# Performance work log

Measured on AMD Instinct MI355X. Metric: run time of the kernel, lower is better.

Reference implementation:

```python
import jax, jax.numpy as jnp
import numpy as np

B, N, C, H = 16, 1029, 1024, 16
D = C // H  # head_dim = 64
N_ROPE = 1024  # patch tokens covered by rope; prefix = N - N_ROPE = 5


def setup_inputs() -> dict:
    key = jax.random.key(0)
    ks = jax.random.split(key, 8)
    x = jax.random.normal(ks[0], (B, N, C), dtype=jnp.float32)
    rope_sin = jax.random.uniform(ks[1], (N_ROPE, D), dtype=jnp.float32, minval=-1.0, maxval=1.0)
    rope_cos = jax.random.uniform(ks[2], (N_ROPE, D), dtype=jnp.float32, minval=-1.0, maxval=1.0)
    s = 1.0 / np.sqrt(C)
    W_qkv = jax.random.normal(ks[3], (3 * C, C), dtype=jnp.float32) * s
    b_qkv = jax.random.normal(ks[4], (3 * C,), dtype=jnp.float32) * 0.02
    W_proj = jax.random.normal(ks[5], (C, C), dtype=jnp.float32) * s
    b_proj = jax.random.normal(ks[6], (C,), dtype=jnp.float32) * 0.02
    return {"x": x, "rope_sin": rope_sin, "rope_cos": rope_cos,
            "W_qkv": W_qkv, "b_qkv": b_qkv, "W_proj": W_proj, "b_proj": b_proj}


def _rotate_half(t):
    t1, t2 = jnp.split(t, 2, axis=-1)
    return jnp.concatenate([-t2, t1], axis=-1)


def _rope_apply(t, sin, cos):
    # t: [B, H, N_rope, D]; sin/cos: [N_rope, D] broadcast over B, H
    return t * cos + _rotate_half(t) * sin


def reference(x, rope_sin, rope_cos, W_qkv, b_qkv, W_proj, b_proj):
    b, n, c = x.shape
    h, d = H, c // H
    # QKV projection (torch Linear: x @ W.T + b)
    qkv = x @ W_qkv.T + b_qkv                       # [B, N, 3C]
    qkv = qkv.reshape(b, n, 3, h, d)
    q = jnp.transpose(qkv[:, :, 0], (0, 2, 1, 3))   # [B, H, N, D]
    k = jnp.transpose(qkv[:, :, 1], (0, 2, 1, 3))
    v = jnp.transpose(qkv[:, :, 2], (0, 2, 1, 3))
    # RoPE on the patch-token suffix only
    prefix = n - rope_sin.shape[-2]
    q = jnp.concatenate([q[:, :, :prefix], _rope_apply(q[:, :, prefix:], rope_sin, rope_cos)], axis=2)
    k = jnp.concatenate([k[:, :, :prefix], _rope_apply(k[:, :, prefix:], rope_sin, rope_cos)], axis=2)
    # Scaled dot-product attention (default scale = 1/sqrt(D))
    scale = 1.0 / jnp.sqrt(jnp.asarray(d, dtype=x.dtype))
    scores = jnp.einsum('bhqd,bhkd->bhqk', q, k) * scale
    attn = jax.nn.softmax(scores, axis=-1)
    out = jnp.einsum('bhqk,bhkd->bhqd', attn, v)    # [B, H, N, D]
    out = jnp.transpose(out, (0, 2, 1, 3)).reshape(b, n, c)
    # Output projection
    return out @ W_proj.T + b_proj
```

## Files before the change

kernel.cpp:

```cpp
#include <hip/hip_runtime.h>
#include <cfloat>
#include <math.h>

#define B_      16
#define N_TOK   1029
#define C_      1024
#define H_      16
#define D_      64
#define PREFIX  5
#define M_ROWS  (B_ * N_TOK)
#define HEAD_SLAB ((size_t)B_ * H_ * N_TOK * D_)
#define VT_STRIDE 1088

typedef __attribute__((ext_vector_type(8))) short bf16x8;
typedef __attribute__((ext_vector_type(4))) float f32x4;

__device__ __forceinline__ unsigned short f2bf(float f) {
    unsigned u = __float_as_uint(f);
    u += 0x7fffu + ((u >> 16) & 1u);
    return (unsigned short)(u >> 16);
}
__device__ __forceinline__ float bf2f(unsigned short h) {
    return __uint_as_float(((unsigned)h) << 16);
}

__global__ __launch_bounds__(256)
void split_kernel(const float* __restrict__ in, unsigned short* __restrict__ hi,
                  unsigned short* __restrict__ lo, int n4)
{
    const int i = blockIdx.x * 256 + threadIdx.x;
    if (i >= n4) return;
    const float4 v = ((const float4*)in)[i];
    ushort4 h, l;
    h.x = f2bf(v.x); l.x = f2bf(v.x - bf2f(h.x));
    h.y = f2bf(v.y); l.y = f2bf(v.y - bf2f(h.y));
    h.z = f2bf(v.z); l.z = f2bf(v.z - bf2f(h.z));
    h.w = f2bf(v.w); l.w = f2bf(v.w - bf2f(h.w));
    ((ushort4*)hi)[i] = h;
    ((ushort4*)lo)[i] = l;
}

__global__ __launch_bounds__(256)
void gemm_mfma(const unsigned short* __restrict__ Ahi, const unsigned short* __restrict__ Alo,
               const unsigned short* __restrict__ Whi, const unsigned short* __restrict__ Wlo,
               const float* __restrict__ bias, float* __restrict__ out,
               int M, int Ncols, int K, int scatter)
{
    __shared__ unsigned short lds[4][128 * 32];

    const int tid  = threadIdx.x;
    const int wave = tid >> 6;
    const int lane = tid & 63;
    const int bx = blockIdx.x, by = blockIdx.y;
    const int wm = wave >> 1, wn = wave & 1;

    f32x4 acc[4][4];
#pragma unroll
    for (int mi = 0; mi < 4; ++mi)
#pragma unroll
        for (int ni = 0; ni < 4; ++ni)
            acc[mi][ni] = (f32x4){0.f, 0.f, 0.f, 0.f};

    const unsigned short* src = (wave == 0) ? Ahi : (wave == 1) ? Alo
                              : (wave == 2) ? Whi : Wlo;
    const bool isA  = (wave < 2);
    const int  row0 = isA ? by * 128 : bx * 128;
    const int  rlo  = lane >> 2;
    const int  koff = (lane & 3) << 3;

    const int lm = lane & 15;
    const int q8 = (lane >> 4) << 3;

    for (int k0 = 0; k0 < K; k0 += 32) {
        __syncthreads();
#pragma unroll
        for (int i = 0; i < 8; ++i) {
            int grow = row0 + i * 16 + rlo;
            if (isA && grow > M - 1) grow = M - 1;
            const unsigned short* g = src + (size_t)grow * K + k0 + koff;
            __builtin_amdgcn_global_load_lds(
                (__attribute__((address_space(1))) void*)g,
                (__attribute__((address_space(3))) void*)&lds[wave][i * 512],
                16, 0, 0);
        }
        __syncthreads();

        bf16x8 ah[4], al[4], bh[4], bl[4];
#pragma unroll
        for (int mi = 0; mi < 4; ++mi) {
            const int r = wm * 64 + mi * 16 + lm;
            ah[mi] = *(const bf16x8*)&lds[0][r * 32 + q8];
            al[mi] = *(const bf16x8*)&lds[1][r * 32 + q8];
        }
#pragma unroll
        for (int ni = 0; ni < 4; ++ni) {
            const int r = wn * 64 + ni * 16 + lm;
            bh[ni] = *(const bf16x8*)&lds[2][r * 32 + q8];
            bl[ni] = *(const bf16x8*)&lds[3][r * 32 + q8];
        }
#pragma unroll
        for (int mi = 0; mi < 4; ++mi)
#pragma unroll
            for (int ni = 0; ni < 4; ++ni) {
                acc[mi][ni] = __builtin_amdgcn_mfma_f32_16x16x32_bf16(ah[mi], bh[ni], acc[mi][ni], 0, 0, 0);
                acc[mi][ni] = __builtin_amdgcn_mfma_f32_16x16x32_bf16(ah[mi], bl[ni], acc[mi][ni], 0, 0, 0);
                acc[mi][ni] = __builtin_amdgcn_mfma_f32_16x16x32_bf16(al[mi], bh[ni], acc[mi][ni], 0, 0, 0);
            }
    }

    const int quad = lane >> 4;
#pragma unroll
    for (int mi = 0; mi < 4; ++mi) {
#pragma unroll
        for (int r = 0; r < 4; ++r) {
            const int gm = by * 128 + wm * 64 + mi * 16 + quad * 4 + r;
            if (gm >= M) continue;
            if (!scatter) {
#pragma unroll
                for (int ni = 0; ni < 4; ++ni) {
                    const int gn = bx * 128 + wn * 64 + ni * 16 + lm;
                    out[(size_t)gm * Ncols + gn] = acc[mi][ni][r] + bias[gn];
                }
            } else {
                const int b   = gm / N_TOK;
                const int tok = gm - b * N_TOK;
#pragma unroll
                for (int ni = 0; ni < 4; ++ni) {
                    const int gn    = bx * 128 + wn * 64 + ni * 16 + lm;
                    const int which = gn >> 10;
                    const int h     = (gn >> 6) & 15;
                    const int d     = gn & 63;
                    const size_t dst = (size_t)which * HEAD_SLAB +
                                       (((size_t)(b * H_ + h)) * N_TOK + tok) * 64 + d;
                    out[dst] = acc[mi][ni][r] + bias[gn];
                }
            }
        }
    }
}

__global__ __launch_bounds__(256)
void rope_convert(const float* __restrict__ qf, const float* __restrict__ kf,
                  const float* __restrict__ sin_, const float* __restrict__ cos_,
                  unsigned short* __restrict__ qhi, unsigned short* __restrict__ qlo,
                  unsigned short* __restrict__ khi, unsigned short* __restrict__ klo)
{
    const int idx = blockIdx.x * 256 + threadIdx.x;
    const int total = B_ * H_ * N_TOK * 32;
    if (idx >= total) return;
    const int d   = idx & 31;
    const int tmp = idx >> 5;
    const int n   = tmp % N_TOK;
    const int bh  = tmp / N_TOK;

    const size_t base = ((size_t)bh * N_TOK + n) * 64;
    float q1 = qf[base + d], q2 = qf[base + d + 32];
    float k1 = kf[base + d], k2 = kf[base + d + 32];

    if (n >= PREFIX) {
        const int r = n - PREFIX;
        const float c1 = cos_[r * 64 + d];
        const float c2 = cos_[r * 64 + d + 32];
        const float s1 = sin_[r * 64 + d];
        const float s2 = sin_[r * 64 + d + 32];
        const float nq1 = q1 * c1 - q2 * s1;
        const float nq2 = q2 * c2 + q1 * s2;
        q1 = nq1; q2 = nq2;
        const float nk1 = k1 * c1 - k2 * s1;
        const float nk2 = k2 * c2 + k1 * s2;
        k1 = nk1; k2 = nk2;
    }
    q1 *= 0.125f; q2 *= 0.125f;

    unsigned short h;
    h = f2bf(q1); qhi[base + d]      = h; qlo[base + d]      = f2bf(q1 - bf2f(h));
    h = f2bf(q2); qhi[base + d + 32] = h; qlo[base + d + 32] = f2bf(q2 - bf2f(h));
    h = f2bf(k1); khi[base + d]      = h; klo[base + d]      = f2bf(k1 - bf2f(h));
    h = f2bf(k2); khi[base + d + 32] = h; klo[base + d + 32] = f2bf(k2 - bf2f(h));
}

__global__ __launch_bounds__(256)
void v_transpose(const float* __restrict__ vf, unsigned short* __restrict__ vt)
{
    __shared__ float t[64][65];
    const int tid = threadIdx.x;
    const int kt0 = blockIdx.x * 64;
    const int bh  = blockIdx.y;
    const float* src = vf + (size_t)bh * N_TOK * 64;

#pragma unroll
    for (int p = 0; p < 4; ++p) {
        const int e   = p * 256 + tid;
        const int key = e >> 4;
        const int c4  = (e & 15) << 2;
        const int gk  = kt0 + key;
        float4 v = make_float4(0.f, 0.f, 0.f, 0.f);
        if (gk < N_TOK) v = *(const float4*)(src + (size_t)gk * 64 + c4);
        t[key][c4 + 0] = v.x;
        t[key][c4 + 1] = v.y;
        t[key][c4 + 2] = v.z;
        t[key][c4 + 3] = v.w;
    }
    __syncthreads();

    const int d  = tid >> 2;
    const int kb = (tid & 3) << 4;
    unsigned short buf[16];
#pragma unroll
    for (int j = 0; j < 16; ++j) buf[j] = f2bf(t[kb + j][d]);
    unsigned short* dst = vt + (size_t)bh * 64 * VT_STRIDE + (size_t)d * VT_STRIDE + kt0 + kb;
#pragma unroll
    for (int j = 0; j < 4; ++j)
        *(ushort4*)(dst + j * 4) = *(ushort4*)&buf[j * 4];
}

__global__ __launch_bounds__(256, 2)
void attn_mfma2(const unsigned short* __restrict__ qhi_g, const unsigned short* __restrict__ qlo_g,
                const unsigned short* __restrict__ khi_g, const unsigned short* __restrict__ klo_g,
                const unsigned short* __restrict__ vt_g,
                unsigned short* __restrict__ Ohi, unsigned short* __restrict__ Olo)
{
    __shared__ unsigned short Khl[2][64 * 64];
    __shared__ unsigned short Kll[2][64 * 64];
    __shared__ unsigned short Vtl[2][64 * 64];
    __shared__ unsigned short Pl[128 * 64];

    const int tid  = threadIdx.x;
    const int wave = tid >> 6;
    const int lane = tid & 63;
    const int lm   = lane & 15;
    const int quad = lane >> 4;
    const int bh   = blockIdx.x;
    const int q0   = blockIdx.y * 128;
    const int b    = bh >> 4;
    const int h    = bh & 15;

    const unsigned short* Qh  = qhi_g + (size_t)bh * N_TOK * 64;
    const unsigned short* Ql  = qlo_g + (size_t)bh * N_TOK * 64;
    const unsigned short* Khb = khi_g + (size_t)bh * N_TOK * 64;
    const unsigned short* Klb = klo_g + (size_t)bh * N_TOK * 64;
    const unsigned short* Vtb = vt_g  + (size_t)bh * 64 * VT_STRIDE;

#define STAGE(bs, kt0_) do {                                                     \
    _Pragma("unroll")                                                            \
    for (int pass = 0; pass < 2; ++pass) {                                       \
        const int t  = pass * 256 + tid;                                         \
        const int r  = t >> 3;                                                   \
        const int qs = t & 7;                                                    \
        const int sw = (qs ^ (r & 7)) << 3;                                      \
        const int ldsoff = (pass * 256 + wave * 64) * 8;                         \
        const int gk = min((kt0_) + r, N_TOK - 1);                               \
        __builtin_amdgcn_global_load_lds(                                        \
            (__attribute__((address_space(1))) void*)(Khb + (size_t)gk * 64 + sw), \
            (__attribute__((address_space(3))) void*)&Khl[bs][ldsoff], 16, 0, 0);  \
        __builtin_amdgcn_global_load_lds(                                        \
            (__attribute__((address_space(1))) void*)(Klb + (size_t)gk * 64 + sw), \
            (__attribute__((address_space(3))) void*)&Kll[bs][ldsoff], 16, 0, 0);  \
        __builtin_amdgcn_global_load_lds(                                        \
            (__attribute__((address_space(1))) void*)(Vtb + (size_t)r * VT_STRIDE + (kt0_) + sw), \
            (__attribute__((address_space(3))) void*)&Vtl[bs][ldsoff], 16, 0, 0);  \
    }                                                                            \
} while (0)

    STAGE(0, 0);

    bf16x8 qh[2][2], ql[2][2];
#pragma unroll
    for (int rt = 0; rt < 2; ++rt) {
        int row = q0 + wave * 32 + rt * 16 + lm;
        if (row > N_TOK - 1) row = N_TOK - 1;
#pragma unroll
        for (int s = 0; s < 2; ++s) {
            const size_t off = (size_t)row * 64 + s * 32 + quad * 8;
            qh[rt][s] = *(const bf16x8*)&Qh[off];
            ql[rt][s] = *(const bf16x8*)&Ql[off];
        }
    }

    f32x4 o[2][4];
    float m_i[2][4], l_i[2][4];
#pragma unroll
    for (int rt = 0; rt < 2; ++rt)
#pragma unroll
        for (int r = 0; r < 4; ++r) {
            m_i[rt][r] = -FLT_MAX;
            l_i[rt][r] = 0.f;
            o[rt][r] = (f32x4){0.f, 0.f, 0.f, 0.f};
        }

    asm volatile("s_waitcnt vmcnt(0)\n\ts_barrier" ::: "memory");

    for (int kt = 0; kt < 17; ++kt) {
        const int kt0 = kt * 64;
        const int cur = kt & 1;

        if (kt < 16) STAGE(cur ^ 1, kt0 + 64);

        f32x4 s_acc[2][4];
#pragma unroll
        for (int rt = 0; rt < 2; ++rt)
#pragma unroll
            for (int ct = 0; ct < 4; ++ct)
                s_acc[rt][ct] = (f32x4){0.f, 0.f, 0.f, 0.f};

#pragma unroll
        for (int ct = 0; ct < 4; ++ct) {
            const int krow = ct * 16 + lm;
#pragma unroll
            for (int s = 0; s < 2; ++s) {
                const int chunk = ((s * 4 + quad) ^ (krow & 7)) << 3;
                const bf16x8 kbh = *(const bf16x8*)&Khl[cur][krow * 64 + chunk];
                const bf16x8 kbl = *(const bf16x8*)&Kll[cur][krow * 64 + chunk];
#pragma unroll
                for (int rt = 0; rt < 2; ++rt) {
                    s_acc[rt][ct] = __builtin_amdgcn_mfma_f32_16x16x32_bf16(qh[rt][s], kbh, s_acc[rt][ct], 0, 0, 0);
                    s_acc[rt][ct] = __builtin_amdgcn_mfma_f32_16x16x32_bf16(qh[rt][s], kbl, s_acc[rt][ct], 0, 0, 0);
                    s_acc[rt][ct] = __builtin_amdgcn_mfma_f32_16x16x32_bf16(ql[rt][s], kbh, s_acc[rt][ct], 0, 0, 0);
                }
            }
        }

        if (kt0 + 64 > N_TOK) {
#pragma unroll
            for (int ct = 0; ct < 4; ++ct) {
                if (kt0 + ct * 16 + lm >= N_TOK) {
#pragma unroll
                    for (int rt = 0; rt < 2; ++rt)
#pragma unroll
                        for (int r = 0; r < 4; ++r) s_acc[rt][ct][r] = -FLT_MAX;
                }
            }
        }

#pragma unroll
        for (int rt = 0; rt < 2; ++rt) {
#pragma unroll
            for (int r = 0; r < 4; ++r) {
                float mt = fmaxf(fmaxf(s_acc[rt][0][r], s_acc[rt][1][r]),
                                 fmaxf(s_acc[rt][2][r], s_acc[rt][3][r]));
                mt = fmaxf(mt, __shfl_xor(mt, 1));
                mt = fmaxf(mt, __shfl_xor(mt, 2));
                mt = fmaxf(mt, __shfl_xor(mt, 4));
                mt = fmaxf(mt, __shfl_xor(mt, 8));
                const float mnew  = fmaxf(m_i[rt][r], mt);
                const float alpha = __expf(m_i[rt][r] - mnew);
                float pv[4], rs = 0.f;
#pragma unroll
                for (int ct = 0; ct < 4; ++ct) {
                    pv[ct] = __expf(s_acc[rt][ct][r] - mnew);
                    rs += pv[ct];
                }
                rs += __shfl_xor(rs, 1);
                rs += __shfl_xor(rs, 2);
                rs += __shfl_xor(rs, 4);
                rs += __shfl_xor(rs, 8);
                l_i[rt][r] = l_i[rt][r] * alpha + rs;
                m_i[rt][r] = mnew;
#pragma unroll
                for (int dt = 0; dt < 4; ++dt) o[rt][dt][r] *= alpha;
                const int prow = wave * 32 + rt * 16 + quad * 4 + r;
#pragma unroll
                for (int ct = 0; ct < 4; ++ct) {
                    const int col = ct * 16 + lm;
                    const int idx = prow * 64 + ((((col >> 3) ^ (prow & 7)) << 3) | (col & 7));
                    Pl[idx] = f2bf(pv[ct]);
                }
            }
        }

#pragma unroll
        for (int ks = 0; ks < 2; ++ks) {
            bf16x8 pf[2];
#pragma unroll
            for (int rt = 0; rt < 2; ++rt) {
                const int prow = wave * 32 + rt * 16 + lm;
                const int chunk = ((ks * 4 + quad) ^ (prow & 7)) << 3;
                pf[rt] = *(const bf16x8*)&Pl[prow * 64 + chunk];
            }
#pragma unroll
            for (int dt = 0; dt < 4; ++dt) {
                const int vrow = dt * 16 + lm;
                const int chunk = ((ks * 4 + quad) ^ (vrow & 7)) << 3;
                const bf16x8 vh = *(const bf16x8*)&Vtl[cur][vrow * 64 + chunk];
#pragma unroll
                for (int rt = 0; rt < 2; ++rt)
                    o[rt][dt] = __builtin_amdgcn_mfma_f32_16x16x32_bf16(pf[rt], vh, o[rt][dt], 0, 0, 0);
            }
        }

        asm volatile("s_waitcnt vmcnt(0)\n\ts_barrier" ::: "memory");
    }
#undef STAGE

#pragma unroll
    for (int rt = 0; rt < 2; ++rt) {
#pragma unroll
        for (int r = 0; r < 4; ++r) {
            const int gq = q0 + wave * 32 + rt * 16 + quad * 4 + r;
            if (gq >= N_TOK) continue;
            const float inv = 1.0f / l_i[rt][r];
            const size_t base = (((size_t)(b * N_TOK + gq)) * H_ + h) * D_;
#pragma unroll
            for (int dt = 0; dt < 4; ++dt) {
                const float val = o[rt][dt][r] * inv;
                const unsigned short hb = f2bf(val);
                Ohi[base + dt * 16 + lm] = hb;
                Olo[base + dt * 16 + lm] = f2bf(val - bf2f(hb));
            }
        }
    }
}

extern "C" void kernel_launch(void* const* d_in, const int* in_sizes, int n_in,
                              void* d_out, int out_size, void* d_ws, size_t ws_size,
                              hipStream_t stream)
{
    const float* x        = (const float*)d_in[0];
    const float* rope_sin = (const float*)d_in[1];
    const float* rope_cos = (const float*)d_in[2];
    const float* W_qkv    = (const float*)d_in[3];
    const float* b_qkv    = (const float*)d_in[4];
    const float* W_proj   = (const float*)d_in[5];
    const float* b_proj   = (const float*)d_in[6];
    float* out = (float*)d_out;

    float* q_buf = (float*)d_ws;
    float* k_buf = q_buf + HEAD_SLAB;
    float* v_buf = q_buf + 2 * HEAD_SLAB;
    float* slab4 = q_buf + 3 * HEAD_SLAB;

    unsigned short* x_hi = (unsigned short*)slab4;
    unsigned short* x_lo = x_hi + HEAD_SLAB;
    unsigned short* wq_hi = (unsigned short*)d_out;
    unsigned short* wq_lo = wq_hi + (size_t)3 * C_ * C_;

    unsigned short* vthi  = (unsigned short*)d_out;
    unsigned short* qhi   = (unsigned short*)v_buf;
    unsigned short* qlo   = qhi + HEAD_SLAB;
    unsigned short* khi   = (unsigned short*)slab4;
    unsigned short* klo   = khi + HEAD_SLAB;
    unsigned short* attn_hi = (unsigned short*)q_buf;
    unsigned short* attn_lo = attn_hi + HEAD_SLAB;
    unsigned short* wp_hi = (unsigned short*)k_buf;
    unsigned short* wp_lo = wp_hi + (size_t)C_ * C_;

    {
        const int n4x = M_ROWS * C_ / 4;
        split_kernel<<<(n4x + 255) / 256, 256, 0, stream>>>(x, x_hi, x_lo, n4x);
        const int n4q = 3 * C_ * C_ / 4;
        split_kernel<<<(n4q + 255) / 256, 256, 0, stream>>>(W_qkv, wq_hi, wq_lo, n4q);
    }
    {
        dim3 grid(3 * C_ / 128, (M_ROWS + 127) / 128);
        gemm_mfma<<<grid, 256, 0, stream>>>(x_hi, x_lo, wq_hi, wq_lo, b_qkv,
                                            q_buf, M_ROWS, 3 * C_, C_, 1);
    }
    {
        dim3 grid(17, B_ * H_);
        v_transpose<<<grid, 256, 0, stream>>>(v_buf, vthi);
    }
    {
        const int total = B_ * H_ * N_TOK * 32;
        rope_convert<<<(total + 255) / 256, 256, 0, stream>>>(
            q_buf, k_buf, rope_sin, rope_cos, qhi, qlo, khi, klo);
    }
    {
        dim3 grid(B_ * H_, (N_TOK + 127) / 128);
        attn_mfma2<<<grid, 256, 0, stream>>>(qhi, qlo, khi, klo, vthi,
                                             attn_hi, attn_lo);
    }
    {
        const int n4p = C_ * C_ / 4;
        split_kernel<<<(n4p + 255) / 256, 256, 0, stream>>>(W_proj, wp_hi, wp_lo, n4p);
    }
    {
        dim3 grid(C_ / 128, (M_ROWS + 127) / 128);
        gemm_mfma<<<grid, 256, 0, stream>>>(attn_hi, attn_lo, wp_hi, wp_lo, b_proj,
                                            out, M_ROWS, C_, C_, 0);
    }
}
```

Baseline: 976.8 us.

## Rewrite split-bf16 GEMM with 256x256 tiles, double-buffered async LDS loads and swizzle

Replaces the 128x128, 4-wave GEMM with a 256x256, 8-wave kernel. It double-buffers LDS and issues global_load_lds for the next K-tile in stages, interleaved with the three MFMA passes (hi*hi, hi*lo, lo*hi), using vmcnt waits and barriers. It also adds an XOR swizzle to LDS fragment reads to avoid bank conflicts and raises wave priority during MFMA bursts. The aim is to hide global load latency and raise operand reuse. In exchange it uses 128KB of LDS and more accumulator registers, and the larger tiles leave fewer blocks for the grid (the M tail is wasted).

```diff
diff --git a/kernel.cpp b/kernel.cpp
--- a/kernel.cpp
+++ b/kernel.cpp
@@ -40,104 +40,146 @@
     ((ushort4*)lo)[i] = l;
 }
 
-__global__ __launch_bounds__(256)
-void gemm_mfma(const unsigned short* __restrict__ Ahi, const unsigned short* __restrict__ Alo,
-               const unsigned short* __restrict__ Whi, const unsigned short* __restrict__ Wlo,
-               const float* __restrict__ bias, float* __restrict__ out,
-               int M, int Ncols, int K, int scatter)
+__device__ __forceinline__ bf16x8 frag_ld(const unsigned short* slab, int r, int q) {
+    const int L = r >> 1;
+    const int s = (q | ((r & 1) << 2)) ^ (L & 7);
+    return *(const bf16x8*)(slab + L * 64 + s * 8);
+}
+
+#define WAIT_BAR(N) do {                                          \
+    asm volatile("s_waitcnt vmcnt(" #N ")" ::: "memory");         \
+    __builtin_amdgcn_s_barrier();                                 \
+    __builtin_amdgcn_sched_barrier(0);                            \
+} while (0)
+
+__global__ __launch_bounds__(512, 2)
+void gemm_mfma8(const unsigned short* __restrict__ Ahi, const unsigned short* __restrict__ Alo,
+                const unsigned short* __restrict__ Whi, const unsigned short* __restrict__ Wlo,
+                const float* __restrict__ bias, float* __restrict__ out,
+                int M, int Ncols, int K, int scatter)
 {
-    __shared__ unsigned short lds[4][128 * 32];
+    __shared__ unsigned short lds[2][4][256 * 32];
 
     const int tid  = threadIdx.x;
     const int wave = tid >> 6;
     const int lane = tid & 63;
+    const int lm   = lane & 15;
+    const int quad = lane >> 4;
     const int bx = blockIdx.x, by = blockIdx.y;
-    const int wm = wave >> 1, wn = wave & 1;
-
-    f32x4 acc[4][4];
-#pragma unroll
-    for (int mi = 0; mi < 4; ++mi)
+    const int wm = wave >> 2;
+    const int wn = wave & 3;
+    const int rowA = by * 256;
+    const int rowB = bx * 256;
+
+    f32x4 acc[8][4];
+#pragma unroll
+    for (int mi = 0; mi < 8; ++mi)
 #pragma unroll
         for (int ni = 0; ni < 4; ++ni)
             acc[mi][ni] = (f32x4){0.f, 0.f, 0.f, 0.f};
 
-    const unsigned short* src = (wave == 0) ? Ahi : (wave == 1) ? Alo
-                              : (wave == 2) ? Whi : Wlo;
-    const bool isA  = (wave < 2);
-    const int  row0 = isA ? by * 128 : bx * 128;
-    const int  rlo  = lane >> 2;
-    const int  koff = (lane & 3) << 3;
-
-    const int lm = lane & 15;
-    const int q8 = (lane >> 4) << 3;
-
-    for (int k0 = 0; k0 < K; k0 += 32) {
-        __syncthreads();
-#pragma unroll
-        for (int i = 0; i < 8; ++i) {
-            int grow = row0 + i * 16 + rlo;
-            if (isA && grow > M - 1) grow = M - 1;
-            const unsigned short* g = src + (size_t)grow * K + k0 + koff;
-            __builtin_amdgcn_global_load_lds(
-                (__attribute__((address_space(1))) void*)g,
-                (__attribute__((address_space(3))) void*)&lds[wave][i * 512],
-                16, 0, 0);
-        }
-        __syncthreads();
-
-        bf16x8 ah[4], al[4], bh[4], bl[4];
-#pragma unroll
-        for (int mi = 0; mi < 4; ++mi) {
-            const int r = wm * 64 + mi * 16 + lm;
-            ah[mi] = *(const bf16x8*)&lds[0][r * 32 + q8];
-            al[mi] = *(const bf16x8*)&lds[1][r * 32 + q8];
-        }
+#define STAGE(buf_, slab_, base_, row0_, doClamp_, k0_) do {                          \
+    _Pragma("unroll")                                                                 \
+    for (int i_ = 0; i_ < 2; ++i_) {                                                  \
+        const int c_ = i_ * 512 + tid;                                                \
+        const int L_ = c_ >> 3;                                                       \
+        const int u_ = (c_ & 7) ^ (L_ & 7);                                           \
+        int grow_ = (row0_) + 2 * L_ + (u_ >> 2);                                     \
+        if (doClamp_) grow_ = min(grow_, M - 1);                                      \
+        const unsigned short* src_ = (base_) + (size_t)grow_ * K + (k0_) + (u_ & 3) * 8; \
+        __builtin_amdgcn_global_load_lds(                                             \
+            (__attribute__((address_space(1))) void*)src_,                            \
+            (__attribute__((address_space(3))) void*)&lds[buf_][slab_][(i_ * 512 + wave * 64) * 8], \
+            16, 0, 0);                                                                \
+    }                                                                                 \
+} while (0)
+
+    STAGE(0, 0, Ahi, rowA, true,  0);
+    STAGE(0, 2, Whi, rowB, false, 0);
+    STAGE(0, 3, Wlo, rowB, false, 0);
+    STAGE(0, 1, Alo, rowA, true,  0);
+
+    const int NT = K >> 5;
+    for (int t = 0; t < NT; ++t) {
+        const int cur = t & 1, nxt = cur ^ 1;
+        const int tn = (t + 1 == NT) ? 0 : t + 1;
+        const int k1 = tn << 5;
+
+        WAIT_BAR(4);
+        STAGE(nxt, 0, Ahi, rowA, true,  k1);
+        STAGE(nxt, 2, Whi, rowB, false, k1);
+        bf16x8 b[4], a[8];
+#pragma unroll
+        for (int ni = 0; ni < 4; ++ni)
+            b[ni] = frag_ld(&lds[cur][2][0], wn * 64 + ni * 16 + lm, quad);
+#pragma unroll
+        for (int mi = 0; mi < 8; ++mi)
+            a[mi] = frag_ld(&lds[cur][0][0], wm * 128 + mi * 16 + lm, quad);
+        __builtin_amdgcn_s_setprio(1);
+#pragma unroll
+        for (int mi = 0; mi < 8; ++mi)
+#pragma unroll
+            for (int ni = 0; ni < 4; ++ni)
+                acc[mi][ni] = __builtin_amdgcn_mfma_f32_16x16x32_bf16(a[mi], b[ni], acc[mi][ni], 0, 0, 0);
+        __builtin_amdgcn_s_setprio(0);
+
+        WAIT_BAR(6);
+        STAGE(nxt, 3, Wlo, rowB, false, k1);
+        __builtin_amdgcn_s_setprio(1);
 #pragma unroll
         for (int ni = 0; ni < 4; ++ni) {
-            const int r = wn * 64 + ni * 16 + lm;
-            bh[ni] = *(const bf16x8*)&lds[2][r * 32 + q8];
-            bl[ni] = *(const bf16x8*)&lds[3][r * 32 + q8];
-        }
-#pragma unroll
-        for (int mi = 0; mi < 4; ++mi)
-#pragma unroll
-            for (int ni = 0; ni < 4; ++ni) {
-                acc[mi][ni] = __builtin_amdgcn_mfma_f32_16x16x32_bf16(ah[mi], bh[ni], acc[mi][ni], 0, 0, 0);
-                acc[mi][ni] = __builtin_amdgcn_mfma_f32_16x16x32_bf16(ah[mi], bl[ni], acc[mi][ni], 0, 0, 0);
-                acc[mi][ni] = __builtin_amdgcn_mfma_f32_16x16x32_bf16(al[mi], bh[ni], acc[mi][ni], 0, 0, 0);
-            }
-    }
-
-    const int quad = lane >> 4;
-#pragma unroll
-    for (int mi = 0; mi < 4; ++mi) {
-#pragma unroll
-        for (int r = 0; r < 4; ++r) {
-            const int gm = by * 128 + wm * 64 + mi * 16 + quad * 4 + r;
+            const bf16x8 bl = frag_ld(&lds[cur][3][0], wn * 64 + ni * 16 + lm, quad);
+#pragma unroll
+            for (int mi = 0; mi < 8; ++mi)
+                acc[mi][ni] = __builtin_amdgcn_mfma_f32_16x16x32_bf16(a[mi], bl, acc[mi][ni], 0, 0, 0);
+        }
+        __builtin_amdgcn_s_setprio(0);
+
+        WAIT_BAR(6);
+        STAGE(nxt, 1, Alo, rowA, true, k1);
+        __builtin_amdgcn_s_setprio(1);
+#pragma unroll
+        for (int mi = 0; mi < 8; ++mi) {
+            const bf16x8 al = frag_ld(&lds[cur][1][0], wm * 128 + mi * 16 + lm, quad);
+#pragma unroll
+            for (int ni = 0; ni < 4; ++ni)
+                acc[mi][ni] = __builtin_amdgcn_mfma_f32_16x16x32_bf16(al, b[ni], acc[mi][ni], 0, 0, 0);
+        }
+        __builtin_amdgcn_s_setprio(0);
+    }
+#undef STAGE
+    asm volatile("s_waitcnt vmcnt(0)" ::: "memory");
+
+#pragma unroll
+    for (int mi = 0; mi < 8; ++mi) {
+#pragma unroll
+        for (int rr = 0; rr < 4; ++rr) {
+            const int gm = rowA + wm * 128 + mi * 16 + quad * 4 + rr;
             if (gm >= M) continue;
             if (!scatter) {
 #pragma unroll
                 for (int ni = 0; ni < 4; ++ni) {
-                    const int gn = bx * 128 + wn * 64 + ni * 16 + lm;
-                    out[(size_t)gm * Ncols + gn] = acc[mi][ni][r] + bias[gn];
+                    const int gn = rowB + wn * 64 + ni * 16 + lm;
+                    out[(size_t)gm * Ncols + gn] = acc[mi][ni][rr] + bias[gn];
                 }
             } else {
-                const int b   = gm / N_TOK;
-                const int tok = gm - b * N_TOK;
+                const int b_  = gm / N_TOK;
+                const int tok = gm - b_ * N_TOK;
 #pragma unroll
                 for (int ni = 0; ni < 4; ++ni) {
-                    const int gn    = bx * 128 + wn * 64 + ni * 16 + lm;
+                    const int gn    = rowB + wn * 64 + ni * 16 + lm;
                     const int which = gn >> 10;
                     const int h     = (gn >> 6) & 15;
                     const int d     = gn & 63;
                     const size_t dst = (size_t)which * HEAD_SLAB +
-                                       (((size_t)(b * H_ + h)) * N_TOK + tok) * 64 + d;
-                    out[dst] = acc[mi][ni][r] + bias[gn];
+                                       (((size_t)(b_ * H_ + h)) * N_TOK + tok) * 64 + d;
+                    out[dst] = acc[mi][ni][rr] + bias[gn];
                 }
             }
         }
     }
 }
+#undef WAIT_BAR
 
 __global__ __launch_bounds__(256)
 void rope_convert(const float* __restrict__ qf, const float* __restrict__ kf,
@@ -451,9 +493,9 @@
         split_kernel<<<(n4q + 255) / 256, 256, 0, stream>>>(W_qkv, wq_hi, wq_lo, n4q);
     }
     {
-        dim3 grid(3 * C_ / 128, (M_ROWS + 127) / 128);
-        gemm_mfma<<<grid, 256, 0, stream>>>(x_hi, x_lo, wq_hi, wq_lo, b_qkv,
-                                            q_buf, M_ROWS, 3 * C_, C_, 1);
+        dim3 grid(3 * C_ / 256, (M_ROWS + 255) / 256);
+        gemm_mfma8<<<grid, 512, 0, stream>>>(x_hi, x_lo, wq_hi, wq_lo, b_qkv,
+                                             q_buf, M_ROWS, 3 * C_, C_, 1);
     }
     {
         dim3 grid(17, B_ * H_);
@@ -474,8 +516,8 @@
         split_kernel<<<(n4p + 255) / 256, 256, 0, stream>>>(W_proj, wp_hi, wp_lo, n4p);
     }
     {
-        dim3 grid(C_ / 128, (M_ROWS + 127) / 128);
-        gemm_mfma<<<grid, 256, 0, stream>>>(attn_hi, attn_lo, wp_hi, wp_lo, b_proj,
-                                            out, M_ROWS, C_, C_, 0);
-    }
-}
+        dim3 grid(C_ / 256, (M_ROWS + 255) / 256);
+        gemm_mfma8<<<grid, 512, 0, stream>>>(attn_hi, attn_lo, wp_hi, wp_lo, b_proj,
+                                             out, M_ROWS, C_, C_, 0);
+    }
+}
```

New measurement: 944.8 us. 3.3% less time.
